# Kernel optimization log

Hardware: AMD Instinct MI355X
Metric: run time of the kernel (lower is better)

## Reference

```python
import jax, jax.numpy as jnp
import numpy as np

B, N, D = 8, 512, 3


def setup_inputs() -> dict:
    key = jax.random.key(0)
    ks = jax.random.split(key, 9)
    s = lambda fan_in: 1.0 / np.sqrt(fan_in)
    return {
        "coords": jax.random.normal(ks[0], (B, N, D), jnp.float32),
        "fw0": jax.random.normal(ks[1], (3, 64), jnp.float32) * s(3),
        "fb0": jnp.zeros((64,), jnp.float32),
        "fw1": jax.random.normal(ks[2], (64, 128), jnp.float32) * s(64),
        "fb1": jnp.zeros((128,), jnp.float32),
        "aw0": jax.random.normal(ks[3], (6, 64), jnp.float32) * s(6),
        "ab0": jnp.zeros((64,), jnp.float32),
        "aw1": jax.random.normal(ks[4], (64, 64), jnp.float32) * s(64),
        "ab1": jnp.zeros((64,), jnp.float32),
        "aw2": jax.random.normal(ks[5], (64, 1), jnp.float32) * s(64),
        "ab2": jnp.zeros((1,), jnp.float32),
        "uw0": jax.random.normal(ks[6], (259, 256), jnp.float32) * s(259),
        "ub0": jnp.zeros((256,), jnp.float32),
        "uw1": jax.random.normal(ks[7], (256, 128), jnp.float32) * s(256),
        "ub1": jnp.zeros((128,), jnp.float32),
    }


def reference(coords, fw0, fb0, fw1, fb1, aw0, ab0, aw1, ab1, aw2, ab2,
              uw0, ub0, uw1, ub1):
    relu = jax.nn.relu
    # node feature MLP: (B, N, 3) -> (B, N, 128)
    h = relu(relu(coords @ fw0 + fb0) @ fw1 + fb1)
    # pairwise concat: (B, N, N, 2D)
    nP = coords.shape[1]
    pi = jnp.broadcast_to(coords[:, :, None, :], (B, nP, nP, D))
    pj = jnp.broadcast_to(coords[:, None, :, :], (B, nP, nP, D))
    pair = jnp.concatenate([pi, pj], axis=-1)
    # adjacency MLP -> scalar per pair; note final layer also has relu
    a = relu(pair @ aw0 + ab0)
    a = relu(a @ aw1 + ab1)
    A = relu(a @ aw2 + ab2)[..., 0]  # (B, N, N)
    # aggregate
    V = jnp.matmul(A, h)  # (B, N, 128)
    updates = jnp.concatenate([h, coords, V], axis=-1)  # (B, N, 259)
    h_next = relu(relu(updates @ uw0 + ub0) @ uw1 + ub1)
    # max pool over points
    return jnp.max(h_next, axis=1)  # (B, 128)
```

## Files before the change

### kernel.cpp

```cpp
#include <hip/hip_runtime.h>
#include <hip/hip_bf16.h>

#define B_ 8
#define N_ 512

typedef __attribute__((ext_vector_type(8))) __bf16 bf16x8;
typedef __attribute__((ext_vector_type(8))) _Float16 f16x8;
typedef __attribute__((ext_vector_type(4))) _Float16 f16x4;
typedef __attribute__((ext_vector_type(2))) _Float16 h2;
typedef __attribute__((ext_vector_type(4))) float f32x4;
typedef __attribute__((ext_vector_type(4))) unsigned int u32x4;
typedef __attribute__((ext_vector_type(2))) unsigned int u32x2;

__device__ __forceinline__ unsigned pk_bf16(float hi, float lo) {
    return __builtin_amdgcn_perm(__builtin_bit_cast(unsigned, hi),
                                 __builtin_bit_cast(unsigned, lo), 0x07060302u);
}

__device__ __forceinline__ h2 pkrtz(float a, float b) {
    return __builtin_bit_cast(h2, __builtin_amdgcn_cvt_pkrtz(a, b));
}
__device__ __forceinline__ unsigned pkrtz_u(float a, float b) {
    return __builtin_bit_cast(unsigned, __builtin_amdgcn_cvt_pkrtz(a, b));
}
__device__ __forceinline__ unsigned relu2_u(h2 v) {
    const h2 z2 = {(_Float16)0.0f, (_Float16)0.0f};
    return __builtin_bit_cast(unsigned, __builtin_elementwise_max(v, z2));
}

__global__ __launch_bounds__(256) void k_mega(
    const float* __restrict__ coords,
    const float* __restrict__ fw0, const float* __restrict__ fb0,
    const float* __restrict__ fw1, const float* __restrict__ fb1,
    const float* __restrict__ aw0, const float* __restrict__ ab0,
    const float* __restrict__ aw1, const float* __restrict__ ab1,
    const float* __restrict__ aw2, const float* __restrict__ ab2,
    const float* __restrict__ uw0, const float* __restrict__ uw1,
    __bf16* __restrict__ h_bf, __bf16* __restrict__ h_t,
    __bf16* __restrict__ w0t, __bf16* __restrict__ w1t,
    __bf16* __restrict__ A,
    float* __restrict__ out, int out_size)
{
    const int blk = blockIdx.x;
    const int t = threadIdx.x;

    if (blk < 1024) {
        __shared__ __align__(16) _Float16 s_aw1p[4096];
        __shared__ __align__(16) float s_w[576];
        __shared__ __align__(8) unsigned s_cj[512][2];

        const int b = blk >> 7;

        {
            f32x4 wv[4];
#pragma unroll
            for (int p = 0; p < 4; ++p)
                wv[p] = *(const f32x4*)(aw1 + t * 16 + p * 4);
            const int row = t >> 2;
            const int ct = t & 3;
            const int s = row >> 5;
            const int qq = (row >> 3) & 3;
            const int j = row & 7;
            const int base = s * 2048 + ct * 512 + qq * 128 + j;
#pragma unroll
            for (int e = 0; e < 16; ++e)
                s_aw1p[base + e * 8] = (_Float16)wv[e >> 2][e & 3];

            if (t < 144) {
                const int o = t * 4;
                f32x4 v;
                if (o < 384)      v = *(const f32x4*)(aw0 + o);
                else if (o < 448) v = *(const f32x4*)(ab0 + (o - 384));
                else if (o < 512) v = *(const f32x4*)(aw2 + (o - 448));
                else              v = *(const f32x4*)(ab1 + (o - 512));
                *(f32x4*)&s_w[o] = v;
            }

            const float* cb = coords + (size_t)b * N_ * 3;
#pragma unroll
            for (int jj = t; jj < 512; jj += 256) {
                const float* cj = cb + jj * 3;
                s_cj[jj][0] = pkrtz_u(cj[0], cj[1]);
                s_cj[jj][1] = pkrtz_u(cj[2], 1.0f);
            }
        }
        __syncthreads();

        const int l = t & 63;
        const int wave = t >> 6;
        const int q = l >> 4;
        const int m = l & 15;
        const int i = ((blk & 127) << 2) + wave;

        const float* ci = coords + (size_t)(b * N_ + i) * 3;
        const float ci0 = ci[0], ci1 = ci[1], ci2 = ci[2];

        f16x4 a0f[4];
        {
            const int chb = ((m >> 2) << 3) + (m & 3);
            const int offs[4] = {0, 4, 32, 36};
#pragma unroll
            for (int t4 = 0; t4 < 4; ++t4) {
                const int ch = chb + offs[t4];
                float w3 = s_w[192 + ch], w4 = s_w[256 + ch], w5 = s_w[320 + ch];
                float o = s_w[384 + ch] + ci0 * s_w[ch] + ci1 * s_w[64 + ch]
                                        + ci2 * s_w[128 + ch];
                u32x2 fr;
                fr[0] = (q == 0) ? pkrtz_u(w3, w4) : 0u;
                fr[1] = (q == 0) ? pkrtz_u(w5, o) : 0u;
                a0f[t4] = __builtin_bit_cast(f16x4, fr);
            }
        }

        f16x4 ewf[4];
#pragma unroll
        for (int ct = 0; ct < 4; ++ct) {
            const float* ep = &s_w[448 + ct * 16 + (q << 2)];
            u32x2 fr;
            fr[0] = pkrtz_u(ep[0], ep[1]);
            fr[1] = pkrtz_u(ep[2], ep[3]);
            ewf[ct] = __builtin_bit_cast(f16x4, fr);
        }

        f16x8 bfr[2][4];
#pragma unroll
        for (int s = 0; s < 2; ++s)
#pragma unroll
            for (int ct = 0; ct < 4; ++ct)
                bfr[s][ct] = *(const f16x8*)&s_aw1p[s * 2048 + ct * 512 + q * 128 + m * 8];

        f32x4 ab1q[4];
#pragma unroll
        for (int ct = 0; ct < 4; ++ct)
            ab1q[ct] = *(const f32x4*)&s_w[512 + ct * 16 + (q << 2)];

        const float ab2s = ab2[0];
        const f32x4 pr0 = {ab2s, ab2s, ab2s, ab2s};
        const f32x4 zf = {0.f, 0.f, 0.f, 0.f};

        __bf16* Arow = A + ((size_t)(b * N_ + i) << 9);

#pragma unroll 2
        for (int tt = 0; tt < 32; ++tt) {
            f16x4 bj = __builtin_bit_cast(f16x4, *(const u32x2*)s_cj[(tt << 4) + m]);

            f32x4 d0 = __builtin_amdgcn_mfma_f32_16x16x16f16(a0f[0], bj, zf, 0, 0, 0);
            f32x4 d1 = __builtin_amdgcn_mfma_f32_16x16x16f16(a0f[1], bj, zf, 0, 0, 0);
            f32x4 d2 = __builtin_amdgcn_mfma_f32_16x16x16f16(a0f[2], bj, zf, 0, 0, 0);
            f32x4 d3 = __builtin_amdgcn_mfma_f32_16x16x16f16(a0f[3], bj, zf, 0, 0, 0);

            u32x4 pa, pb;
            pa[0] = relu2_u(pkrtz(d0[0], d0[1]));
            pa[1] = relu2_u(pkrtz(d0[2], d0[3]));
            pa[2] = relu2_u(pkrtz(d1[0], d1[1]));
            pa[3] = relu2_u(pkrtz(d1[2], d1[3]));
            pb[0] = relu2_u(pkrtz(d2[0], d2[1]));
            pb[1] = relu2_u(pkrtz(d2[2], d2[3]));
            pb[2] = relu2_u(pkrtz(d3[0], d3[1]));
            pb[3] = relu2_u(pkrtz(d3[2], d3[3]));
            f16x8 a0 = __builtin_bit_cast(f16x8, pa);
            f16x8 a1 = __builtin_bit_cast(f16x8, pb);

            f32x4 c0v = __builtin_amdgcn_mfma_f32_16x16x32_f16(bfr[0][0], a0, ab1q[0], 0, 0, 0);
            c0v = __builtin_amdgcn_mfma_f32_16x16x32_f16(bfr[1][0], a1, c0v, 0, 0, 0);
            f32x4 c1v = __builtin_amdgcn_mfma_f32_16x16x32_f16(bfr[0][1], a0, ab1q[1], 0, 0, 0);
            c1v = __builtin_amdgcn_mfma_f32_16x16x32_f16(bfr[1][1], a1, c1v, 0, 0, 0);
            f32x4 c2v = __builtin_amdgcn_mfma_f32_16x16x32_f16(bfr[0][2], a0, ab1q[2], 0, 0, 0);
            c2v = __builtin_amdgcn_mfma_f32_16x16x32_f16(bfr[1][2], a1, c2v, 0, 0, 0);
            f32x4 c3v = __builtin_amdgcn_mfma_f32_16x16x32_f16(bfr[0][3], a0, ab1q[3], 0, 0, 0);
            c3v = __builtin_amdgcn_mfma_f32_16x16x32_f16(bfr[1][3], a1, c3v, 0, 0, 0);

            u32x2 r0, r1, r2, r3;
            r0[0] = relu2_u(pkrtz(c0v[0], c0v[1]));
            r0[1] = relu2_u(pkrtz(c0v[2], c0v[3]));
            r1[0] = relu2_u(pkrtz(c1v[0], c1v[1]));
            r1[1] = relu2_u(pkrtz(c1v[2], c1v[3]));
            r2[0] = relu2_u(pkrtz(c2v[0], c2v[1]));
            r2[1] = relu2_u(pkrtz(c2v[2], c2v[3]));
            r3[0] = relu2_u(pkrtz(c3v[0], c3v[1]));
            r3[1] = relu2_u(pkrtz(c3v[2], c3v[3]));

            f32x4 pra = __builtin_amdgcn_mfma_f32_16x16x16f16(
                ewf[0], __builtin_bit_cast(f16x4, r0), pr0, 0, 0, 0);
            pra = __builtin_amdgcn_mfma_f32_16x16x16f16(
                ewf[1], __builtin_bit_cast(f16x4, r1), pra, 0, 0, 0);
            f32x4 prb = __builtin_amdgcn_mfma_f32_16x16x16f16(
                ewf[2], __builtin_bit_cast(f16x4, r2), zf, 0, 0, 0);
            prb = __builtin_amdgcn_mfma_f32_16x16x16f16(
                ewf[3], __builtin_bit_cast(f16x4, r3), prb, 0, 0, 0);

            if (l < 16) Arow[(tt << 4) + l] = (__bf16)fmaxf(pra[0] + prb[0], 0.0f);
        }
    } else if (blk < 2048) {
        const int row0 = (blk - 1024) << 2;
        const int b = row0 >> 9;
        const int n0 = row0 & 511;
        __shared__ float cds4[4][4];
        __shared__ float hid4[4][64];
        if (t < 12) {
            int r = t / 3, d = t - 3 * r;
            cds4[r][d] = coords[(size_t)row0 * 3 + t];
        }
        __syncthreads();
        {
            int r = t >> 6, ch = t & 63;
            float v = fb0[ch];
            v += cds4[r][0] * fw0[0 * 64 + ch];
            v += cds4[r][1] * fw0[1 * 64 + ch];
            v += cds4[r][2] * fw0[2 * 64 + ch];
            hid4[r][ch] = fmaxf(v, 0.0f);
        }
        __syncthreads();
        {
            int ch = t & 127;
            int rp = (t >> 7) << 1;
            float hv0 = fb1[ch], hv1 = hv0;
#pragma unroll 4
            for (int k = 0; k < 64; ++k) {
                float w = fw1[k * 128 + ch];
                hv0 += hid4[rp][k] * w;
                hv1 += hid4[rp + 1][k] * w;
            }
            hv0 = fmaxf(hv0, 0.0f);
            hv1 = fmaxf(hv1, 0.0f);
            h_bf[((size_t)(row0 + rp) << 7) + ch] = (__bf16)hv0;
            h_bf[((size_t)(row0 + rp + 1) << 7) + ch] = (__bf16)hv1;
            *(unsigned*)(h_t + (size_t)(b * 128 + ch) * 512 + n0 + rp) =
                pk_bf16(hv1, hv0);
        }
    } else if (blk < 2304) {
        int k = blk - 2048;
        int c = t;
        int src = (k < 128) ? k : (k + 3);
        w0t[(size_t)c * 256 + k] = (__bf16)uw0[(size_t)src * 256 + c];
    } else if (blk < 2432) {
        int id = (blk - 2304) * 256 + t;
        int c = id & 127, k = id >> 7;
        w1t[(size_t)c * 256 + k] = (__bf16)uw1[(size_t)k * 128 + c];
    } else {
        int i = (blk - 2432) * 256 + t;
        if (i < out_size) out[i] = 0.0f;
    }
}

__global__ __launch_bounds__(1024) void k_aggupd(
    const __bf16* __restrict__ A, const __bf16* __restrict__ h_t,
    const __bf16* __restrict__ h_bf, const float* __restrict__ coords,
    const float* __restrict__ uw0, const float* __restrict__ ub0,
    const __bf16* __restrict__ w0t, const __bf16* __restrict__ w1t,
    const float* __restrict__ ub1,
    float* __restrict__ out)
{
    const int t = threadIdx.x;
    const int w = t >> 6;
    const int gw = w & 7;
    const int ks = w >> 3;
    const int l = t & 63;
    const int q = l >> 4;
    const int m = l & 15;
    const int row0 = blockIdx.x << 4;
    const int b = row0 >> 9;

    __shared__ __align__(16) __bf16 act[16][264];
    __shared__ __align__(16) __bf16 u1[16][264];
    __shared__ float vp[2][16][128];
    __shared__ float cds[16][4];

    {
        unsigned hv = *(const unsigned*)(h_bf + ((size_t)row0 << 7) + t * 2);
        *(unsigned*)&act[(t * 2) >> 7][(t * 2) & 127] = hv;
    }
    if (t < 48) {
        int r = t / 3, d = t - 3 * r;
        cds[r][d] = coords[(size_t)row0 * 3 + t];
    }

    const __bf16* Ar = A + (size_t)(row0 + m) * 512 + ks * 256 + q * 8;
    const __bf16* hp = h_t + ((size_t)b << 16) + (size_t)(gw * 16 + m) * 512
                       + ks * 256 + q * 8;
    f32x4 acc = {0.f, 0.f, 0.f, 0.f};
#pragma unroll 4
    for (int kt = 0; kt < 8; ++kt) {
        bf16x8 av = *(const bf16x8*)(Ar + kt * 32);
        bf16x8 bv = *(const bf16x8*)(hp + kt * 32);
        acc = __builtin_amdgcn_mfma_f32_16x16x32_bf16(av, bv, acc, 0, 0, 0);
    }
#pragma unroll
    for (int r = 0; r < 4; ++r)
        vp[ks][q * 4 + r][gw * 16 + m] = acc[r];
    __syncthreads();

#pragma unroll
    for (int it = 0; it < 2; ++it) {
        int idx = t + it * 1024;
        int row = idx >> 7, ch = idx & 127;
        act[row][128 + ch] = (__bf16)(vp[0][row][ch] + vp[1][row][ch]);
    }
    __syncthreads();

    bf16x8 af[8];
#pragma unroll
    for (int ch = 0; ch < 8; ++ch)
        af[ch] = *(const bf16x8*)&act[m][q * 8 + 32 * ch];
    {
        const int c = w * 16 + m;
        const float wx = uw0[128 * 256 + c];
        const float wy = uw0[129 * 256 + c];
        const float wz = uw0[130 * 256 + c];
        const float bias = ub0[c];
        f32x4 a1c;
#pragma unroll
        for (int r = 0; r < 4; ++r)
            a1c[r] = bias + cds[q * 4 + r][0] * wx + cds[q * 4 + r][1] * wy
                          + cds[q * 4 + r][2] * wz;
        const __bf16* wp = w0t + (size_t)c * 256 + q * 8;
#pragma unroll
        for (int ch = 0; ch < 8; ++ch) {
            bf16x8 bfr = *(const bf16x8*)(wp + 32 * ch);
            a1c = __builtin_amdgcn_mfma_f32_16x16x32_bf16(af[ch], bfr, a1c, 0, 0, 0);
        }
#pragma unroll
        for (int r = 0; r < 4; ++r)
            u1[q * 4 + r][c] = (__bf16)fmaxf(a1c[r], 0.0f);
    }
    __syncthreads();

    if (w < 8) {
        bf16x8 af2[8];
#pragma unroll
        for (int ch = 0; ch < 8; ++ch)
            af2[ch] = *(const bf16x8*)&u1[m][q * 8 + 32 * ch];
        const int c = w * 16 + m;
        float bias = ub1[c];
        f32x4 a2c = {bias, bias, bias, bias};
        const __bf16* wp = w1t + (size_t)c * 256 + q * 8;
#pragma unroll
        for (int ch = 0; ch < 8; ++ch) {
            bf16x8 bfr = *(const bf16x8*)(wp + 32 * ch);
            a2c = __builtin_amdgcn_mfma_f32_16x16x32_bf16(af2[ch], bfr, a2c, 0, 0, 0);
        }
        float mx = fmaxf(fmaxf(a2c[0], a2c[1]), fmaxf(a2c[2], a2c[3]));
        mx = fmaxf(mx, 0.0f);
        mx = fmaxf(mx, __shfl_xor(mx, 16, 64));
        mx = fmaxf(mx, __shfl_xor(mx, 32, 64));
        if (l < 16)
            atomicMax((int*)(out + ((size_t)b << 7) + c), __float_as_int(mx));
    }
}

extern "C" void kernel_launch(void* const* d_in, const int* in_sizes, int n_in,
                              void* d_out, int out_size, void* d_ws, size_t ws_size,
                              hipStream_t stream)
{
    const float* coords = (const float*)d_in[0];
    const float* fw0 = (const float*)d_in[1];
    const float* fb0 = (const float*)d_in[2];
    const float* fw1 = (const float*)d_in[3];
    const float* fb1 = (const float*)d_in[4];
    const float* aw0 = (const float*)d_in[5];
    const float* ab0 = (const float*)d_in[6];
    const float* aw1 = (const float*)d_in[7];
    const float* ab1 = (const float*)d_in[8];
    const float* aw2 = (const float*)d_in[9];
    const float* ab2 = (const float*)d_in[10];
    const float* uw0 = (const float*)d_in[11];
    const float* ub0 = (const float*)d_in[12];
    const float* uw1 = (const float*)d_in[13];
    const float* ub1 = (const float*)d_in[14];
    float* out = (float*)d_out;

    char* ws = (char*)d_ws;
    __bf16* A    = (__bf16*)(ws);
    __bf16* h_t  = (__bf16*)(ws + (4u << 20));
    __bf16* h_bf = (__bf16*)(ws + (5u << 20));
    __bf16* w0t  = (__bf16*)(ws + (6u << 20));
    __bf16* w1t  = (__bf16*)(ws + (6u << 20) + (128u << 10));

    k_mega<<<2436, 256, 0, stream>>>(coords, fw0, fb0, fw1, fb1,
                                     aw0, ab0, aw1, ab1, aw2, ab2, uw0, uw1,
                                     h_bf, h_t, w0t, w1t, A, out, out_size);
    k_aggupd<<<256, 1024, 0, stream>>>(A, h_t, h_bf, coords, uw0, ub0,
                                       w0t, w1t, ub1, out);
}
```

Measured before the change: 129.7 us.

## Process two rows per wave over half the columns in the adjacency MLP

Each wave of the adjacency-MLP blocks now handles two query points i over a 256-column half of j, instead of one point over all 512 columns. The block count stays the same. This gives two independent MFMA chains per iteration for more instruction-level parallelism, and halves the shared coordinate staging per block. It also software-prefetches the next j fragment from LDS and writes two rows of output per store instruction, at the cost of more live registers and a non-unrolled loop.

```diff
diff --git a/kernel.cpp b/kernel.cpp
--- a/kernel.cpp
+++ b/kernel.cpp
@@ -47,9 +47,12 @@
     if (blk < 1024) {
         __shared__ __align__(16) _Float16 s_aw1p[4096];
         __shared__ __align__(16) float s_w[576];
-        __shared__ __align__(8) unsigned s_cj[512][2];
+        __shared__ __align__(8) unsigned s_cj[256][2];
 
         const int b = blk >> 7;
+        const int rest = blk & 127;
+        const int jh = rest & 1;
+        const int ig = rest >> 1;
 
         {
             f32x4 wv[4];
@@ -76,13 +79,9 @@
                 *(f32x4*)&s_w[o] = v;
             }
 
-            const float* cb = coords + (size_t)b * N_ * 3;
-#pragma unroll
-            for (int jj = t; jj < 512; jj += 256) {
-                const float* cj = cb + jj * 3;
-                s_cj[jj][0] = pkrtz_u(cj[0], cj[1]);
-                s_cj[jj][1] = pkrtz_u(cj[2], 1.0f);
-            }
+            const float* cj = coords + (size_t)(b * N_ + jh * 256 + t) * 3;
+            s_cj[t][0] = pkrtz_u(cj[0], cj[1]);
+            s_cj[t][1] = pkrtz_u(cj[2], 1.0f);
         }
         __syncthreads();
 
@@ -90,12 +89,13 @@
         const int wave = t >> 6;
         const int q = l >> 4;
         const int m = l & 15;
-        const int i = ((blk & 127) << 2) + wave;
-
-        const float* ci = coords + (size_t)(b * N_ + i) * 3;
-        const float ci0 = ci[0], ci1 = ci[1], ci2 = ci[2];
-
-        f16x4 a0f[4];
+        const int i0 = ig * 8 + wave * 2;
+
+        const float* cp = coords + (size_t)(b * N_ + i0) * 3;
+        const float cA0 = cp[0], cA1 = cp[1], cA2 = cp[2];
+        const float cB0 = cp[3], cB1 = cp[4], cB2 = cp[5];
+
+        f16x4 a0fA[4], a0fB[4];
         {
             const int chb = ((m >> 2) << 3) + (m & 3);
             const int offs[4] = {0, 4, 32, 36};
@@ -103,12 +103,18 @@
             for (int t4 = 0; t4 < 4; ++t4) {
                 const int ch = chb + offs[t4];
                 float w3 = s_w[192 + ch], w4 = s_w[256 + ch], w5 = s_w[320 + ch];
-                float o = s_w[384 + ch] + ci0 * s_w[ch] + ci1 * s_w[64 + ch]
-                                        + ci2 * s_w[128 + ch];
-                u32x2 fr;
-                fr[0] = (q == 0) ? pkrtz_u(w3, w4) : 0u;
-                fr[1] = (q == 0) ? pkrtz_u(w5, o) : 0u;
-                a0f[t4] = __builtin_bit_cast(f16x4, fr);
+                float w0v = s_w[ch], w1v = s_w[64 + ch], w2v = s_w[128 + ch];
+                float bch = s_w[384 + ch];
+                float oA = bch + cA0 * w0v + cA1 * w1v + cA2 * w2v;
+                float oB = bch + cB0 * w0v + cB1 * w1v + cB2 * w2v;
+                unsigned w34 = (q == 0) ? pkrtz_u(w3, w4) : 0u;
+                u32x2 fa, fb;
+                fa[0] = w34;
+                fa[1] = (q == 0) ? pkrtz_u(w5, oA) : 0u;
+                fb[0] = w34;
+                fb[1] = (q == 0) ? pkrtz_u(w5, oB) : 0u;
+                a0fA[t4] = __builtin_bit_cast(f16x4, fa);
+                a0fB[t4] = __builtin_bit_cast(f16x4, fb);
             }
         }
 
@@ -138,58 +144,105 @@
         const f32x4 pr0 = {ab2s, ab2s, ab2s, ab2s};
         const f32x4 zf = {0.f, 0.f, 0.f, 0.f};
 
-        __bf16* Arow = A + ((size_t)(b * N_ + i) << 9);
-
-#pragma unroll 2
-        for (int tt = 0; tt < 32; ++tt) {
-            f16x4 bj = __builtin_bit_cast(f16x4, *(const u32x2*)s_cj[(tt << 4) + m]);
-
-            f32x4 d0 = __builtin_amdgcn_mfma_f32_16x16x16f16(a0f[0], bj, zf, 0, 0, 0);
-            f32x4 d1 = __builtin_amdgcn_mfma_f32_16x16x16f16(a0f[1], bj, zf, 0, 0, 0);
-            f32x4 d2 = __builtin_amdgcn_mfma_f32_16x16x16f16(a0f[2], bj, zf, 0, 0, 0);
-            f32x4 d3 = __builtin_amdgcn_mfma_f32_16x16x16f16(a0f[3], bj, zf, 0, 0, 0);
-
-            u32x4 pa, pb;
-            pa[0] = relu2_u(pkrtz(d0[0], d0[1]));
-            pa[1] = relu2_u(pkrtz(d0[2], d0[3]));
-            pa[2] = relu2_u(pkrtz(d1[0], d1[1]));
-            pa[3] = relu2_u(pkrtz(d1[2], d1[3]));
-            pb[0] = relu2_u(pkrtz(d2[0], d2[1]));
-            pb[1] = relu2_u(pkrtz(d2[2], d2[3]));
-            pb[2] = relu2_u(pkrtz(d3[0], d3[1]));
-            pb[3] = relu2_u(pkrtz(d3[2], d3[3]));
-            f16x8 a0 = __builtin_bit_cast(f16x8, pa);
-            f16x8 a1 = __builtin_bit_cast(f16x8, pb);
-
-            f32x4 c0v = __builtin_amdgcn_mfma_f32_16x16x32_f16(bfr[0][0], a0, ab1q[0], 0, 0, 0);
-            c0v = __builtin_amdgcn_mfma_f32_16x16x32_f16(bfr[1][0], a1, c0v, 0, 0, 0);
-            f32x4 c1v = __builtin_amdgcn_mfma_f32_16x16x32_f16(bfr[0][1], a0, ab1q[1], 0, 0, 0);
-            c1v = __builtin_amdgcn_mfma_f32_16x16x32_f16(bfr[1][1], a1, c1v, 0, 0, 0);
-            f32x4 c2v = __builtin_amdgcn_mfma_f32_16x16x32_f16(bfr[0][2], a0, ab1q[2], 0, 0, 0);
-            c2v = __builtin_amdgcn_mfma_f32_16x16x32_f16(bfr[1][2], a1, c2v, 0, 0, 0);
-            f32x4 c3v = __builtin_amdgcn_mfma_f32_16x16x32_f16(bfr[0][3], a0, ab1q[3], 0, 0, 0);
-            c3v = __builtin_amdgcn_mfma_f32_16x16x32_f16(bfr[1][3], a1, c3v, 0, 0, 0);
-
-            u32x2 r0, r1, r2, r3;
-            r0[0] = relu2_u(pkrtz(c0v[0], c0v[1]));
-            r0[1] = relu2_u(pkrtz(c0v[2], c0v[3]));
-            r1[0] = relu2_u(pkrtz(c1v[0], c1v[1]));
-            r1[1] = relu2_u(pkrtz(c1v[2], c1v[3]));
-            r2[0] = relu2_u(pkrtz(c2v[0], c2v[1]));
-            r2[1] = relu2_u(pkrtz(c2v[2], c2v[3]));
-            r3[0] = relu2_u(pkrtz(c3v[0], c3v[1]));
-            r3[1] = relu2_u(pkrtz(c3v[2], c3v[3]));
-
-            f32x4 pra = __builtin_amdgcn_mfma_f32_16x16x16f16(
-                ewf[0], __builtin_bit_cast(f16x4, r0), pr0, 0, 0, 0);
-            pra = __builtin_amdgcn_mfma_f32_16x16x16f16(
-                ewf[1], __builtin_bit_cast(f16x4, r1), pra, 0, 0, 0);
-            f32x4 prb = __builtin_amdgcn_mfma_f32_16x16x16f16(
-                ewf[2], __builtin_bit_cast(f16x4, r2), zf, 0, 0, 0);
-            prb = __builtin_amdgcn_mfma_f32_16x16x16f16(
-                ewf[3], __builtin_bit_cast(f16x4, r3), prb, 0, 0, 0);
-
-            if (l < 16) Arow[(tt << 4) + l] = (__bf16)fmaxf(pra[0] + prb[0], 0.0f);
+        __bf16* ArowP = A + ((size_t)(b * N_ + i0) << 9) + jh * 256;
+        const int idx0 = ((l >> 4) << 9) + (l & 15);
+
+        u32x2 bjw = *(const u32x2*)s_cj[m];
+
+#pragma unroll 1
+        for (int tt = 0; tt < 16; ++tt) {
+            u32x2 bjn = *(const u32x2*)s_cj[(((tt + 1) & 15) << 4) + m];
+            f16x4 bj = __builtin_bit_cast(f16x4, bjw);
+
+            f32x4 dA0 = __builtin_amdgcn_mfma_f32_16x16x16f16(a0fA[0], bj, zf, 0, 0, 0);
+            f32x4 dA1 = __builtin_amdgcn_mfma_f32_16x16x16f16(a0fA[1], bj, zf, 0, 0, 0);
+            f32x4 dA2 = __builtin_amdgcn_mfma_f32_16x16x16f16(a0fA[2], bj, zf, 0, 0, 0);
+            f32x4 dA3 = __builtin_amdgcn_mfma_f32_16x16x16f16(a0fA[3], bj, zf, 0, 0, 0);
+            f32x4 dB0 = __builtin_amdgcn_mfma_f32_16x16x16f16(a0fB[0], bj, zf, 0, 0, 0);
+            f32x4 dB1 = __builtin_amdgcn_mfma_f32_16x16x16f16(a0fB[1], bj, zf, 0, 0, 0);
+            f32x4 dB2 = __builtin_amdgcn_mfma_f32_16x16x16f16(a0fB[2], bj, zf, 0, 0, 0);
+            f32x4 dB3 = __builtin_amdgcn_mfma_f32_16x16x16f16(a0fB[3], bj, zf, 0, 0, 0);
+
+            u32x4 paA, pbA, paB, pbB;
+            paA[0] = relu2_u(pkrtz(dA0[0], dA0[1]));
+            paA[1] = relu2_u(pkrtz(dA0[2], dA0[3]));
+            paA[2] = relu2_u(pkrtz(dA1[0], dA1[1]));
+            paA[3] = relu2_u(pkrtz(dA1[2], dA1[3]));
+            pbA[0] = relu2_u(pkrtz(dA2[0], dA2[1]));
+            pbA[1] = relu2_u(pkrtz(dA2[2], dA2[3]));
+            pbA[2] = relu2_u(pkrtz(dA3[0], dA3[1]));
+            pbA[3] = relu2_u(pkrtz(dA3[2], dA3[3]));
+            paB[0] = relu2_u(pkrtz(dB0[0], dB0[1]));
+            paB[1] = relu2_u(pkrtz(dB0[2], dB0[3]));
+            paB[2] = relu2_u(pkrtz(dB1[0], dB1[1]));
+            paB[3] = relu2_u(pkrtz(dB1[2], dB1[3]));
+            pbB[0] = relu2_u(pkrtz(dB2[0], dB2[1]));
+            pbB[1] = relu2_u(pkrtz(dB2[2], dB2[3]));
+            pbB[2] = relu2_u(pkrtz(dB3[0], dB3[1]));
+            pbB[3] = relu2_u(pkrtz(dB3[2], dB3[3]));
+            f16x8 a0A = __builtin_bit_cast(f16x8, paA);
+            f16x8 a1A = __builtin_bit_cast(f16x8, pbA);
+            f16x8 a0B = __builtin_bit_cast(f16x8, paB);
+            f16x8 a1B = __builtin_bit_cast(f16x8, pbB);
+
+            f32x4 cA0v = __builtin_amdgcn_mfma_f32_16x16x32_f16(bfr[0][0], a0A, ab1q[0], 0, 0, 0);
+            cA0v = __builtin_amdgcn_mfma_f32_16x16x32_f16(bfr[1][0], a1A, cA0v, 0, 0, 0);
+            f32x4 cA1v = __builtin_amdgcn_mfma_f32_16x16x32_f16(bfr[0][1], a0A, ab1q[1], 0, 0, 0);
+            cA1v = __builtin_amdgcn_mfma_f32_16x16x32_f16(bfr[1][1], a1A, cA1v, 0, 0, 0);
+            f32x4 cA2v = __builtin_amdgcn_mfma_f32_16x16x32_f16(bfr[0][2], a0A, ab1q[2], 0, 0, 0);
+            cA2v = __builtin_amdgcn_mfma_f32_16x16x32_f16(bfr[1][2], a1A, cA2v, 0, 0, 0);
+            f32x4 cA3v = __builtin_amdgcn_mfma_f32_16x16x32_f16(bfr[0][3], a0A, ab1q[3], 0, 0, 0);
+            cA3v = __builtin_amdgcn_mfma_f32_16x16x32_f16(bfr[1][3], a1A, cA3v, 0, 0, 0);
+            f32x4 cB0v = __builtin_amdgcn_mfma_f32_16x16x32_f16(bfr[0][0], a0B, ab1q[0], 0, 0, 0);
+            cB0v = __builtin_amdgcn_mfma_f32_16x16x32_f16(bfr[1][0], a1B, cB0v, 0, 0, 0);
+            f32x4 cB1v = __builtin_amdgcn_mfma_f32_16x16x32_f16(bfr[0][1], a0B, ab1q[1], 0, 0, 0);
+            cB1v = __builtin_amdgcn_mfma_f32_16x16x32_f16(bfr[1][1], a1B, cB1v, 0, 0, 0);
+            f32x4 cB2v = __builtin_amdgcn_mfma_f32_16x16x32_f16(bfr[0][2], a0B, ab1q[2], 0, 0, 0);
+            cB2v = __builtin_amdgcn_mfma_f32_16x16x32_f16(bfr[1][2], a1B, cB2v, 0, 0, 0);
+            f32x4 cB3v = __builtin_amdgcn_mfma_f32_16x16x32_f16(bfr[0][3], a0B, ab1q[3], 0, 0, 0);
+            cB3v = __builtin_amdgcn_mfma_f32_16x16x32_f16(bfr[1][3], a1B, cB3v, 0, 0, 0);
+
+            u32x2 rA0, rA1, rA2, rA3, rB0, rB1, rB2, rB3;
+            rA0[0] = relu2_u(pkrtz(cA0v[0], cA0v[1]));
+            rA0[1] = relu2_u(pkrtz(cA0v[2], cA0v[3]));
+            rA1[0] = relu2_u(pkrtz(cA1v[0], cA1v[1]));
+            rA1[1] = relu2_u(pkrtz(cA1v[2], cA1v[3]));
+            rA2[0] = relu2_u(pkrtz(cA2v[0], cA2v[1]));
+            rA2[1] = relu2_u(pkrtz(cA2v[2], cA2v[3]));
+            rA3[0] = relu2_u(pkrtz(cA3v[0], cA3v[1]));
+            rA3[1] = relu2_u(pkrtz(cA3v[2], cA3v[3]));
+            rB0[0] = relu2_u(pkrtz(cB0v[0], cB0v[1]));
+            rB0[1] = relu2_u(pkrtz(cB0v[2], cB0v[3]));
+            rB1[0] = relu2_u(pkrtz(cB1v[0], cB1v[1]));
+            rB1[1] = relu2_u(pkrtz(cB1v[2], cB1v[3]));
+            rB2[0] = relu2_u(pkrtz(cB2v[0], cB2v[1]));
+            rB2[1] = relu2_u(pkrtz(cB2v[2], cB2v[3]));
+            rB3[0] = relu2_u(pkrtz(cB3v[0], cB3v[1]));
+            rB3[1] = relu2_u(pkrtz(cB3v[2], cB3v[3]));
+
+            f32x4 prAa = __builtin_amdgcn_mfma_f32_16x16x16f16(
+                ewf[0], __builtin_bit_cast(f16x4, rA0), pr0, 0, 0, 0);
+            prAa = __builtin_amdgcn_mfma_f32_16x16x16f16(
+                ewf[1], __builtin_bit_cast(f16x4, rA1), prAa, 0, 0, 0);
+            f32x4 prAb = __builtin_amdgcn_mfma_f32_16x16x16f16(
+                ewf[2], __builtin_bit_cast(f16x4, rA2), zf, 0, 0, 0);
+            prAb = __builtin_amdgcn_mfma_f32_16x16x16f16(
+                ewf[3], __builtin_bit_cast(f16x4, rA3), prAb, 0, 0, 0);
+            f32x4 prBa = __builtin_amdgcn_mfma_f32_16x16x16f16(
+                ewf[0], __builtin_bit_cast(f16x4, rB0), pr0, 0, 0, 0);
+            prBa = __builtin_amdgcn_mfma_f32_16x16x16f16(
+                ewf[1], __builtin_bit_cast(f16x4, rB1), prBa, 0, 0, 0);
+            f32x4 prBb = __builtin_amdgcn_mfma_f32_16x16x16f16(
+                ewf[2], __builtin_bit_cast(f16x4, rB2), zf, 0, 0, 0);
+            prBb = __builtin_amdgcn_mfma_f32_16x16x16f16(
+                ewf[3], __builtin_bit_cast(f16x4, rB3), prBb, 0, 0, 0);
+
+            float vA = prAa[0] + prAb[0];
+            float vB = prBa[0] + prBb[0];
+            float v = (l < 16) ? vA : vB;
+            if (l < 32) ArowP[idx0 + (tt << 4)] = (__bf16)fmaxf(v, 0.0f);
+
+            bjw = bjn;
         }
     } else if (blk < 2048) {
         const int row0 = (blk - 1024) << 2;
```

Result: no change. 130.1 us (+0.3%).

## Fuse adjacency MLP into aggregation kernel, keeping A tile in LDS

Applied to the files above, without the earlier changes.

Moves the pairwise adjacency-MLP computation out of the first kernel and into the aggregation/update kernel. Each 1024-thread block computes its 16 rows of A directly into shared memory instead of writing and rereading the full A matrix through global memory. The final 64->1 projection is merged into two 16x16x32 MFMAs instead of four 16x16x16 ones. The adjacency work now runs on only 256 blocks of 16 waves each, not 1024 blocks of 4 waves. That cuts parallelism for the dominant compute stage and adds LDS pressure, and the tt loop is no longer unrolled.

```diff
diff --git a/kernel.cpp b/kernel.cpp
--- a/kernel.cpp
+++ b/kernel.cpp
@@ -28,171 +28,20 @@
     return __builtin_bit_cast(unsigned, __builtin_elementwise_max(v, z2));
 }
 
-__global__ __launch_bounds__(256) void k_mega(
+__global__ __launch_bounds__(256) void k_prep(
     const float* __restrict__ coords,
     const float* __restrict__ fw0, const float* __restrict__ fb0,
     const float* __restrict__ fw1, const float* __restrict__ fb1,
-    const float* __restrict__ aw0, const float* __restrict__ ab0,
-    const float* __restrict__ aw1, const float* __restrict__ ab1,
-    const float* __restrict__ aw2, const float* __restrict__ ab2,
     const float* __restrict__ uw0, const float* __restrict__ uw1,
     __bf16* __restrict__ h_bf, __bf16* __restrict__ h_t,
     __bf16* __restrict__ w0t, __bf16* __restrict__ w1t,
-    __bf16* __restrict__ A,
     float* __restrict__ out, int out_size)
 {
     const int blk = blockIdx.x;
     const int t = threadIdx.x;
 
     if (blk < 1024) {
-        __shared__ __align__(16) _Float16 s_aw1p[4096];
-        __shared__ __align__(16) float s_w[576];
-        __shared__ __align__(8) unsigned s_cj[512][2];
-
-        const int b = blk >> 7;
-
-        {
-            f32x4 wv[4];
-#pragma unroll
-            for (int p = 0; p < 4; ++p)
-                wv[p] = *(const f32x4*)(aw1 + t * 16 + p * 4);
-            const int row = t >> 2;
-            const int ct = t & 3;
-            const int s = row >> 5;
-            const int qq = (row >> 3) & 3;
-            const int j = row & 7;
-            const int base = s * 2048 + ct * 512 + qq * 128 + j;
-#pragma unroll
-            for (int e = 0; e < 16; ++e)
-                s_aw1p[base + e * 8] = (_Float16)wv[e >> 2][e & 3];
-
-            if (t < 144) {
-                const int o = t * 4;
-                f32x4 v;
-                if (o < 384)      v = *(const f32x4*)(aw0 + o);
-                else if (o < 448) v = *(const f32x4*)(ab0 + (o - 384));
-                else if (o < 512) v = *(const f32x4*)(aw2 + (o - 448));
-                else              v = *(const f32x4*)(ab1 + (o - 512));
-                *(f32x4*)&s_w[o] = v;
-            }
-
-            const float* cb = coords + (size_t)b * N_ * 3;
-#pragma unroll
-            for (int jj = t; jj < 512; jj += 256) {
-                const float* cj = cb + jj * 3;
-                s_cj[jj][0] = pkrtz_u(cj[0], cj[1]);
-                s_cj[jj][1] = pkrtz_u(cj[2], 1.0f);
-            }
-        }
-        __syncthreads();
-
-        const int l = t & 63;
-        const int wave = t >> 6;
-        const int q = l >> 4;
-        const int m = l & 15;
-        const int i = ((blk & 127) << 2) + wave;
-
-        const float* ci = coords + (size_t)(b * N_ + i) * 3;
-        const float ci0 = ci[0], ci1 = ci[1], ci2 = ci[2];
-
-        f16x4 a0f[4];
-        {
-            const int chb = ((m >> 2) << 3) + (m & 3);
-            const int offs[4] = {0, 4, 32, 36};
-#pragma unroll
-            for (int t4 = 0; t4 < 4; ++t4) {
-                const int ch = chb + offs[t4];
-                float w3 = s_w[192 + ch], w4 = s_w[256 + ch], w5 = s_w[320 + ch];
-                float o = s_w[384 + ch] + ci0 * s_w[ch] + ci1 * s_w[64 + ch]
-                                        + ci2 * s_w[128 + ch];
-                u32x2 fr;
-                fr[0] = (q == 0) ? pkrtz_u(w3, w4) : 0u;
-                fr[1] = (q == 0) ? pkrtz_u(w5, o) : 0u;
-                a0f[t4] = __builtin_bit_cast(f16x4, fr);
-            }
-        }
-
-        f16x4 ewf[4];
-#pragma unroll
-        for (int ct = 0; ct < 4; ++ct) {
-            const float* ep = &s_w[448 + ct * 16 + (q << 2)];
-            u32x2 fr;
-            fr[0] = pkrtz_u(ep[0], ep[1]);
-            fr[1] = pkrtz_u(ep[2], ep[3]);
-            ewf[ct] = __builtin_bit_cast(f16x4, fr);
-        }
-
-        f16x8 bfr[2][4];
-#pragma unroll
-        for (int s = 0; s < 2; ++s)
-#pragma unroll
-            for (int ct = 0; ct < 4; ++ct)
-                bfr[s][ct] = *(const f16x8*)&s_aw1p[s * 2048 + ct * 512 + q * 128 + m * 8];
-
-        f32x4 ab1q[4];
-#pragma unroll
-        for (int ct = 0; ct < 4; ++ct)
-            ab1q[ct] = *(const f32x4*)&s_w[512 + ct * 16 + (q << 2)];
-
-        const float ab2s = ab2[0];
-        const f32x4 pr0 = {ab2s, ab2s, ab2s, ab2s};
-        const f32x4 zf = {0.f, 0.f, 0.f, 0.f};
-
-        __bf16* Arow = A + ((size_t)(b * N_ + i) << 9);
-
-#pragma unroll 2
-        for (int tt = 0; tt < 32; ++tt) {
-            f16x4 bj = __builtin_bit_cast(f16x4, *(const u32x2*)s_cj[(tt << 4) + m]);
-
-            f32x4 d0 = __builtin_amdgcn_mfma_f32_16x16x16f16(a0f[0], bj, zf, 0, 0, 0);
-            f32x4 d1 = __builtin_amdgcn_mfma_f32_16x16x16f16(a0f[1], bj, zf, 0, 0, 0);
-            f32x4 d2 = __builtin_amdgcn_mfma_f32_16x16x16f16(a0f[2], bj, zf, 0, 0, 0);
-            f32x4 d3 = __builtin_amdgcn_mfma_f32_16x16x16f16(a0f[3], bj, zf, 0, 0, 0);
-
-            u32x4 pa, pb;
-            pa[0] = relu2_u(pkrtz(d0[0], d0[1]));
-            pa[1] = relu2_u(pkrtz(d0[2], d0[3]));
-            pa[2] = relu2_u(pkrtz(d1[0], d1[1]));
-            pa[3] = relu2_u(pkrtz(d1[2], d1[3]));
-            pb[0] = relu2_u(pkrtz(d2[0], d2[1]));
-            pb[1] = relu2_u(pkrtz(d2[2], d2[3]));
-            pb[2] = relu2_u(pkrtz(d3[0], d3[1]));
-            pb[3] = relu2_u(pkrtz(d3[2], d3[3]));
-            f16x8 a0 = __builtin_bit_cast(f16x8, pa);
-            f16x8 a1 = __builtin_bit_cast(f16x8, pb);
-
-            f32x4 c0v = __builtin_amdgcn_mfma_f32_16x16x32_f16(bfr[0][0], a0, ab1q[0], 0, 0, 0);
-            c0v = __builtin_amdgcn_mfma_f32_16x16x32_f16(bfr[1][0], a1, c0v, 0, 0, 0);
-            f32x4 c1v = __builtin_amdgcn_mfma_f32_16x16x32_f16(bfr[0][1], a0, ab1q[1], 0, 0, 0);
-            c1v = __builtin_amdgcn_mfma_f32_16x16x32_f16(bfr[1][1], a1, c1v, 0, 0, 0);
-            f32x4 c2v = __builtin_amdgcn_mfma_f32_16x16x32_f16(bfr[0][2], a0, ab1q[2], 0, 0, 0);
-            c2v = __builtin_amdgcn_mfma_f32_16x16x32_f16(bfr[1][2], a1, c2v, 0, 0, 0);
-            f32x4 c3v = __builtin_amdgcn_mfma_f32_16x16x32_f16(bfr[0][3], a0, ab1q[3], 0, 0, 0);
-            c3v = __builtin_amdgcn_mfma_f32_16x16x32_f16(bfr[1][3], a1, c3v, 0, 0, 0);
-
-            u32x2 r0, r1, r2, r3;
-            r0[0] = relu2_u(pkrtz(c0v[0], c0v[1]));
-            r0[1] = relu2_u(pkrtz(c0v[2], c0v[3]));
-            r1[0] = relu2_u(pkrtz(c1v[0], c1v[1]));
-            r1[1] = relu2_u(pkrtz(c1v[2], c1v[3]));
-            r2[0] = relu2_u(pkrtz(c2v[0], c2v[1]));
-            r2[1] = relu2_u(pkrtz(c2v[2], c2v[3]));
-            r3[0] = relu2_u(pkrtz(c3v[0], c3v[1]));
-            r3[1] = relu2_u(pkrtz(c3v[2], c3v[3]));
-
-            f32x4 pra = __builtin_amdgcn_mfma_f32_16x16x16f16(
-                ewf[0], __builtin_bit_cast(f16x4, r0), pr0, 0, 0, 0);
-            pra = __builtin_amdgcn_mfma_f32_16x16x16f16(
-                ewf[1], __builtin_bit_cast(f16x4, r1), pra, 0, 0, 0);
-            f32x4 prb = __builtin_amdgcn_mfma_f32_16x16x16f16(
-                ewf[2], __builtin_bit_cast(f16x4, r2), zf, 0, 0, 0);
-            prb = __builtin_amdgcn_mfma_f32_16x16x16f16(
-                ewf[3], __builtin_bit_cast(f16x4, r3), prb, 0, 0, 0);
-
-            if (l < 16) Arow[(tt << 4) + l] = (__bf16)fmaxf(pra[0] + prb[0], 0.0f);
-        }
-    } else if (blk < 2048) {
-        const int row0 = (blk - 1024) << 2;
+        const int row0 = blk << 2;
         const int b = row0 >> 9;
         const int n0 = row0 & 511;
         __shared__ float cds4[4][4];
@@ -228,24 +77,28 @@
             *(unsigned*)(h_t + (size_t)(b * 128 + ch) * 512 + n0 + rp) =
                 pk_bf16(hv1, hv0);
         }
-    } else if (blk < 2304) {
-        int k = blk - 2048;
+    } else if (blk < 1280) {
+        int k = blk - 1024;
         int c = t;
         int src = (k < 128) ? k : (k + 3);
         w0t[(size_t)c * 256 + k] = (__bf16)uw0[(size_t)src * 256 + c];
-    } else if (blk < 2432) {
-        int id = (blk - 2304) * 256 + t;
+    } else if (blk < 1408) {
+        int id = (blk - 1280) * 256 + t;
         int c = id & 127, k = id >> 7;
         w1t[(size_t)c * 256 + k] = (__bf16)uw1[(size_t)k * 128 + c];
     } else {
-        int i = (blk - 2432) * 256 + t;
+        int i = (blk - 1408) * 256 + t;
         if (i < out_size) out[i] = 0.0f;
     }
 }
 
-__global__ __launch_bounds__(1024) void k_aggupd(
-    const __bf16* __restrict__ A, const __bf16* __restrict__ h_t,
-    const __bf16* __restrict__ h_bf, const float* __restrict__ coords,
+#define AP 520
+__global__ __launch_bounds__(1024) void k_fused(
+    const float* __restrict__ coords,
+    const float* __restrict__ aw0, const float* __restrict__ ab0,
+    const float* __restrict__ aw1, const float* __restrict__ ab1,
+    const float* __restrict__ aw2, const float* __restrict__ ab2,
+    const __bf16* __restrict__ h_t, const __bf16* __restrict__ h_bf,
     const float* __restrict__ uw0, const float* __restrict__ ub0,
     const __bf16* __restrict__ w0t, const __bf16* __restrict__ w1t,
     const float* __restrict__ ub1,
@@ -253,41 +106,174 @@
 {
     const int t = threadIdx.x;
     const int w = t >> 6;
-    const int gw = w & 7;
-    const int ks = w >> 3;
     const int l = t & 63;
     const int q = l >> 4;
     const int m = l & 15;
     const int row0 = blockIdx.x << 4;
     const int b = row0 >> 9;
 
+    __shared__ __align__(16) _Float16 s_aw1p[4096];
+    __shared__ __align__(16) float s_w[576];
+    __shared__ __align__(8) unsigned s_cj[512][2];
+    __shared__ __align__(16) __bf16 As[16][AP];
     __shared__ __align__(16) __bf16 act[16][264];
     __shared__ __align__(16) __bf16 u1[16][264];
     __shared__ float vp[2][16][128];
     __shared__ float cds[16][4];
 
     {
+        f32x4 wv = *(const f32x4*)(aw1 + t * 4);
+        const int R = t >> 4;
+        const int C4 = (t & 15) << 2;
+        const int s = R >> 5, qq = (R >> 3) & 3, j = R & 7;
+        const int ct = C4 >> 4, mm0 = C4 & 15;
+        const int base = s * 2048 + ct * 512 + qq * 128 + mm0 * 8 + j;
+#pragma unroll
+        for (int e = 0; e < 4; ++e)
+            s_aw1p[base + e * 8] = (_Float16)wv[e];
+
+        if (t < 144) {
+            const int o = t * 4;
+            f32x4 v;
+            if (o < 384)      v = *(const f32x4*)(aw0 + o);
+            else if (o < 448) v = *(const f32x4*)(ab0 + (o - 384));
+            else if (o < 512) v = *(const f32x4*)(aw2 + (o - 448));
+            else              v = *(const f32x4*)(ab1 + (o - 512));
+            *(f32x4*)&s_w[o] = v;
+        }
+
+        if (t < 512) {
+            const float* cj = coords + ((size_t)b * N_ + t) * 3;
+            s_cj[t][0] = pkrtz_u(cj[0], cj[1]);
+            s_cj[t][1] = pkrtz_u(cj[2], 1.0f);
+        }
+
         unsigned hv = *(const unsigned*)(h_bf + ((size_t)row0 << 7) + t * 2);
         *(unsigned*)&act[(t * 2) >> 7][(t * 2) & 127] = hv;
-    }
-    if (t < 48) {
-        int r = t / 3, d = t - 3 * r;
-        cds[r][d] = coords[(size_t)row0 * 3 + t];
-    }
-
-    const __bf16* Ar = A + (size_t)(row0 + m) * 512 + ks * 256 + q * 8;
-    const __bf16* hp = h_t + ((size_t)b << 16) + (size_t)(gw * 16 + m) * 512
-                       + ks * 256 + q * 8;
-    f32x4 acc = {0.f, 0.f, 0.f, 0.f};
+
+        if (t < 48) {
+            int r = t / 3, d = t - 3 * r;
+            cds[r][d] = coords[(size_t)row0 * 3 + t];
+        }
+    }
+    __syncthreads();
+
+    {
+        const float* cp = coords + (size_t)(row0 + w) * 3;
+        const float ci0 = cp[0], ci1 = cp[1], ci2 = cp[2];
+
+        f16x4 a0f[4];
+        {
+            const int chb = ((m >> 2) << 3) + (m & 3);
+            const int offs[4] = {0, 4, 32, 36};
+#pragma unroll
+            for (int t4 = 0; t4 < 4; ++t4) {
+                const int ch = chb + offs[t4];
+                float o = s_w[384 + ch] + ci0 * s_w[ch] + ci1 * s_w[64 + ch]
+                                        + ci2 * s_w[128 + ch];
+                u32x2 fr;
+                fr[0] = (q == 0) ? pkrtz_u(s_w[192 + ch], s_w[256 + ch]) : 0u;
+                fr[1] = (q == 0) ? pkrtz_u(s_w[320 + ch], o) : 0u;
+                a0f[t4] = __builtin_bit_cast(f16x4, fr);
+            }
+        }
+
+        f16x8 ewf[2];
+#pragma unroll
+        for (int g = 0; g < 2; ++g) {
+            const float* e0 = &s_w[448 + g * 32 + (q << 2)];
+            const float* e1 = e0 + 16;
+            u32x4 fr;
+            fr[0] = pkrtz_u(e0[0], e0[1]);
+            fr[1] = pkrtz_u(e0[2], e0[3]);
+            fr[2] = pkrtz_u(e1[0], e1[1]);
+            fr[3] = pkrtz_u(e1[2], e1[3]);
+            ewf[g] = __builtin_bit_cast(f16x8, fr);
+        }
+
+        f16x8 bfr[2][4];
+#pragma unroll
+        for (int s = 0; s < 2; ++s)
+#pragma unroll
+            for (int ct = 0; ct < 4; ++ct)
+                bfr[s][ct] = *(const f16x8*)&s_aw1p[s * 2048 + ct * 512 + q * 128 + m * 8];
+
+        f32x4 ab1q[4];
+#pragma unroll
+        for (int ct = 0; ct < 4; ++ct)
+            ab1q[ct] = *(const f32x4*)&s_w[512 + ct * 16 + (q << 2)];
+
+        const float ab2s = ab2[0];
+        const f32x4 pr0 = {ab2s, ab2s, ab2s, ab2s};
+        const f32x4 zf = {0.f, 0.f, 0.f, 0.f};
+
+#pragma unroll 1
+        for (int tt = 0; tt < 32; ++tt) {
+            f16x4 bj = __builtin_bit_cast(f16x4, *(const u32x2*)s_cj[(tt << 4) + m]);
+
+            f32x4 d0 = __builtin_amdgcn_mfma_f32_16x16x16f16(a0f[0], bj, zf, 0, 0, 0);
+            f32x4 d1 = __builtin_amdgcn_mfma_f32_16x16x16f16(a0f[1], bj, zf, 0, 0, 0);
+            f32x4 d2 = __builtin_amdgcn_mfma_f32_16x16x16f16(a0f[2], bj, zf, 0, 0, 0);
+            f32x4 d3 = __builtin_amdgcn_mfma_f32_16x16x16f16(a0f[3], bj, zf, 0, 0, 0);
+
+            u32x4 pa, pb;
+            pa[0] = relu2_u(pkrtz(d0[0], d0[1]));
+            pa[1] = relu2_u(pkrtz(d0[2], d0[3]));
+            pa[2] = relu2_u(pkrtz(d1[0], d1[1]));
+            pa[3] = relu2_u(pkrtz(d1[2], d1[3]));
+            pb[0] = relu2_u(pkrtz(d2[0], d2[1]));
+            pb[1] = relu2_u(pkrtz(d2[2], d2[3]));
+            pb[2] = relu2_u(pkrtz(d3[0], d3[1]));
+            pb[3] = relu2_u(pkrtz(d3[2], d3[3]));
+            f16x8 a0 = __builtin_bit_cast(f16x8, pa);
+            f16x8 a1 = __builtin_bit_cast(f16x8, pb);
+
+            f32x4 c0v = __builtin_amdgcn_mfma_f32_16x16x32_f16(bfr[0][0], a0, ab1q[0], 0, 0, 0);
+            c0v = __builtin_amdgcn_mfma_f32_16x16x32_f16(bfr[1][0], a1, c0v, 0, 0, 0);
+            f32x4 c1v = __builtin_amdgcn_mfma_f32_16x16x32_f16(bfr[0][1], a0, ab1q[1], 0, 0, 0);
+            c1v = __builtin_amdgcn_mfma_f32_16x16x32_f16(bfr[1][1], a1, c1v, 0, 0, 0);
+            f32x4 c2v = __builtin_amdgcn_mfma_f32_16x16x32_f16(bfr[0][2], a0, ab1q[2], 0, 0, 0);
+            c2v = __builtin_amdgcn_mfma_f32_16x16x32_f16(bfr[1][2], a1, c2v, 0, 0, 0);
+            f32x4 c3v = __builtin_amdgcn_mfma_f32_16x16x32_f16(bfr[0][3], a0, ab1q[3], 0, 0, 0);
+            c3v = __builtin_amdgcn_mfma_f32_16x16x32_f16(bfr[1][3], a1, c3v, 0, 0, 0);
+
+            u32x4 B0, B1;
+            B0[0] = relu2_u(pkrtz(c0v[0], c0v[1]));
+            B0[1] = relu2_u(pkrtz(c0v[2], c0v[3]));
+            B0[2] = relu2_u(pkrtz(c1v[0], c1v[1]));
+            B0[3] = relu2_u(pkrtz(c1v[2], c1v[3]));
+            B1[0] = relu2_u(pkrtz(c2v[0], c2v[1]));
+            B1[1] = relu2_u(pkrtz(c2v[2], c2v[3]));
+            B1[2] = relu2_u(pkrtz(c3v[0], c3v[1]));
+            B1[3] = relu2_u(pkrtz(c3v[2], c3v[3]));
+
+            f32x4 pr = __builtin_amdgcn_mfma_f32_16x16x32_f16(
+                ewf[0], __builtin_bit_cast(f16x8, B0), pr0, 0, 0, 0);
+            pr = __builtin_amdgcn_mfma_f32_16x16x32_f16(
+                ewf[1], __builtin_bit_cast(f16x8, B1), pr, 0, 0, 0);
+
+            if (l < 16) As[w][(tt << 4) + l] = (__bf16)fmaxf(pr[0], 0.0f);
+        }
+    }
+    __syncthreads();
+
+    const int gw = w & 7;
+    const int ks = w >> 3;
+    {
+        const __bf16* hp = h_t + ((size_t)b << 16) + (size_t)(gw * 16 + m) * 512
+                           + ks * 256 + q * 8;
+        const __bf16* Ar = &As[m][ks * 256 + q * 8];
+        f32x4 acc = {0.f, 0.f, 0.f, 0.f};
 #pragma unroll 4
-    for (int kt = 0; kt < 8; ++kt) {
-        bf16x8 av = *(const bf16x8*)(Ar + kt * 32);
-        bf16x8 bv = *(const bf16x8*)(hp + kt * 32);
-        acc = __builtin_amdgcn_mfma_f32_16x16x32_bf16(av, bv, acc, 0, 0, 0);
-    }
-#pragma unroll
-    for (int r = 0; r < 4; ++r)
-        vp[ks][q * 4 + r][gw * 16 + m] = acc[r];
+        for (int kt = 0; kt < 8; ++kt) {
+            bf16x8 av = *(const bf16x8*)(Ar + kt * 32);
+            bf16x8 bv = *(const bf16x8*)(hp + kt * 32);
+            acc = __builtin_amdgcn_mfma_f32_16x16x32_bf16(av, bv, acc, 0, 0, 0);
+        }
+#pragma unroll
+        for (int r = 0; r < 4; ++r)
+            vp[ks][q * 4 + r][gw * 16 + m] = acc[r];
+    }
     __syncthreads();
 
 #pragma unroll
@@ -370,15 +356,13 @@
     float* out = (float*)d_out;
 
     char* ws = (char*)d_ws;
-    __bf16* A    = (__bf16*)(ws);
-    __bf16* h_t  = (__bf16*)(ws + (4u << 20));
-    __bf16* h_bf = (__bf16*)(ws + (5u << 20));
-    __bf16* w0t  = (__bf16*)(ws + (6u << 20));
-    __bf16* w1t  = (__bf16*)(ws + (6u << 20) + (128u << 10));
-
-    k_mega<<<2436, 256, 0, stream>>>(coords, fw0, fb0, fw1, fb1,
-                                     aw0, ab0, aw1, ab1, aw2, ab2, uw0, uw1,
-                                     h_bf, h_t, w0t, w1t, A, out, out_size);
-    k_aggupd<<<256, 1024, 0, stream>>>(A, h_t, h_bf, coords, uw0, ub0,
-                                       w0t, w1t, ub1, out);
-}
+    __bf16* h_t  = (__bf16*)(ws);
+    __bf16* h_bf = (__bf16*)(ws + (1u << 20));
+    __bf16* w0t  = (__bf16*)(ws + (2u << 20));
+    __bf16* w1t  = (__bf16*)(ws + (2u << 20) + (128u << 10));
+
+    k_prep<<<1412, 256, 0, stream>>>(coords, fw0, fb0, fw1, fb1, uw0, uw1,
+                                     h_bf, h_t, w0t, w1t, out, out_size);
+    k_fused<<<256, 1024, 0, stream>>>(coords, aw0, ab0, aw1, ab1, aw2, ab2,
+                                      h_t, h_bf, uw0, ub0, w0t, w1t, ub1, out);
+}
```

Measured after the change: 122.4 us. -5.7%, faster.
